# Optimization experiments

Hardware: AMD Instinct MI355X
Metric: run time of the kernel (lower is better)

Reference implementation:

```python
import jax, jax.numpy as jnp
from jax import lax
import numpy as np

WINDOW_SIZES = (1, 2, 3)


def _proj(x, w1, b1, w2, b2):
    # gated projection: sigmoid(Linear1) * tanh(Linear2)
    return jax.nn.sigmoid(x @ w1.T + b1) * jnp.tanh(x @ w2.T + b2)


def setup_inputs() -> dict:
    key = jax.random.key(0)
    ks = jax.random.split(key, 16)
    V, E, D = 50000, 1024, 1024
    N, La, Lq = 64, 512, 64
    s = 0.02  # weight scale to keep sigmoid/tanh unsaturated
    return {
        "data_q": jax.random.randint(ks[0], (Lq,), 0, V),
        "data_as": jax.random.randint(ks[1], (N, La), 0, V),
        "emb": jax.random.normal(ks[2], (V, E), jnp.float32),
        "w1": jax.random.normal(ks[3], (D, E), jnp.float32) * s,
        "b1": jnp.zeros((D,), jnp.float32),
        "w2": jax.random.normal(ks[4], (D, E), jnp.float32) * s,
        "b2": jnp.zeros((D,), jnp.float32),
        "cw1": jax.random.normal(ks[5], (D, D, 1), jnp.float32) * s,
        "cb1": jnp.zeros((D,), jnp.float32),
        "cw2": jax.random.normal(ks[6], (D, D, 2), jnp.float32) * s,
        "cb2": jnp.zeros((D,), jnp.float32),
        "cw3": jax.random.normal(ks[7], (D, D, 3), jnp.float32) * s,
        "cb3": jnp.zeros((D,), jnp.float32),
        "lin_w": jax.random.normal(ks[8], (D, 3 * D), jnp.float32) * s,
        "lin_b": jnp.zeros((D,), jnp.float32),
        "soft_w": jax.random.normal(ks[9], (1, D), jnp.float32) * s,
        "soft_b": jnp.zeros((1,), jnp.float32),
    }


def reference(data_q, data_as, emb, w1, b1, w2, b2,
              cw1, cb1, cw2, cb2, cw3, cb3, lin_w, lin_b, soft_w, soft_b):
    N, La = data_as.shape
    a_tok = data_as.reshape(-1)                     # [T] concatenated answers
    emb_a = emb[a_tok]                              # [T, E]
    emb_q = emb[data_q]                             # [Lq, E]
    pa = _proj(emb_a, w1, b1, w2, b2)               # [T, D]
    pq = _proj(emb_q, w1, b1, w2, b2)               # [Lq, D]

    # attention: M_r = q @ a^T ; alpha = softmax over question positions
    M = pq @ pa.T                                   # [Lq, T]
    alpha = jax.nn.softmax(M.T, axis=1)             # [T, Lq]
    Y = alpha @ pq                                  # [T, D]
    sim = pa * Y                                    # elementwise compare (mul)

    starts = jnp.arange(N) * La
    x = sim.T[None]                                 # [1, D, T]
    pools = []
    for w, cw, cb in zip(WINDOW_SIZES, (cw1, cw2, cw3), (cb1, cb2, cb3)):
        conv = lax.conv_general_dilated(
            x, cw, (1,), 'VALID',
            dimension_numbers=('NCW', 'OIW', 'NCW'))[0].T + cb  # [T-w+1, D]
        conv = jax.nn.relu(conv)
        # DMax: per-answer max over rows [start_k, start_k + La - w + 1)
        idx = starts[:, None] + jnp.arange(La - w + 1)[None, :]  # [N, La-w+1]
        pools.append(conv[idx].max(axis=1))          # [N, D]

    cat = jnp.concatenate(pools, axis=1)            # [N, 3D]
    h = jnp.tanh(cat @ lin_w.T + lin_b)             # [N, D]
    logits = (h @ soft_w.T + soft_b).reshape(-1)    # [N]
    return jax.nn.log_softmax(logits)
```

## Files before the change

### kernel.cpp

```cpp
#include <hip/hip_runtime.h>

#define DEV __device__ __forceinline__

typedef __bf16 bf16x8 __attribute__((ext_vector_type(8)));
typedef float f32x4 __attribute__((ext_vector_type(4)));
typedef unsigned short u16;
typedef u16 u16x4 __attribute__((ext_vector_type(4)));

constexpr int T_ANS = 32768;
constexpr int LQ    = 64;
constexpr int M_ALL = T_ANS + LQ;
constexpr int M_PAD = 32896;
constexpr int DIM   = 1024;

DEV u16 f2bf(float x) {
  unsigned u = __float_as_uint(x);
  return (u16)((u + 0x7FFFu + ((u >> 16) & 1u)) >> 16);
}
DEV float bf2f(u16 s) { return __uint_as_float(((unsigned)s) << 16); }

DEV void gl2lds16(const void* g, void* l) {
  __builtin_amdgcn_global_load_lds(
      (const __attribute__((address_space(1))) unsigned int*)g,
      (__attribute__((address_space(3))) unsigned int*)l, 16, 0, 0);
}


__global__ void cast4(const float* __restrict__ src, u16* __restrict__ dst, int n4) {
  int i = blockIdx.x * 256 + threadIdx.x;
  if (i < n4) {
    float4 v = ((const float4*)src)[i];
    u16x4 o = { f2bf(v.x), f2bf(v.y), f2bf(v.z), f2bf(v.w) };
    ((u16x4*)dst)[i] = o;
  }
}

template<int W>
__global__ void cast_conv_w(const float* __restrict__ src, u16* __restrict__ dst) {
  int i = blockIdx.x * 256 + threadIdx.x;
  if (i < 1024 * 1024) {
#pragma unroll
    for (int k = 0; k < W; ++k)
      dst[(size_t)k * (1024 * 1024) + i] = f2bf(src[(size_t)i * W + k]);
  }
}

__global__ void gather_cast(const int* __restrict__ dq, const int* __restrict__ das,
                            const float* __restrict__ emb, u16* __restrict__ X) {
  const int row = blockIdx.x;
  const int c   = threadIdx.x;
  size_t dsto = (size_t)row * DIM + c * 4;
  if (row >= M_ALL) {
    u16x4 z = {0, 0, 0, 0};
    *(u16x4*)(X + dsto) = z;
    return;
  }
  const int tok = (row < T_ANS) ? das[row] : dq[row - T_ANS];
  float4 v = ((const float4*)(emb + (size_t)tok * DIM))[c];
  u16x4 o = { f2bf(v.x), f2bf(v.y), f2bf(v.z), f2bf(v.w) };
  *(u16x4*)(X + dsto) = o;
}

__global__ void transpose_pq(const u16* __restrict__ pa, u16* __restrict__ pqT) {
  int i = blockIdx.x * 256 + threadIdx.x;
  int e = i >> 6, q = i & 63;
  pqT[i] = pa[(size_t)(T_ANS + q) * DIM + e];
}

__global__ void zero_pad_sim(u16* __restrict__ sim) {
  int i = blockIdx.x * 256 + threadIdx.x;
  if (i < 2 * DIM) sim[(size_t)T_ANS * DIM + i] = 0;
}

__global__ void cast_cat(const float* __restrict__ cat, u16* __restrict__ catb) {
  int i = blockIdx.x * 256 + threadIdx.x;
  if (i < 128 * 3072) {
    int row = i / 3072;
    catb[i] = (row < 64) ? f2bf(cat[i]) : (u16)0;
  }
}


__global__ __launch_bounds__(256, 2)
void proj_dual(const u16* __restrict__ X, const u16* __restrict__ B1,
               const u16* __restrict__ B2, const float* __restrict__ b1,
               const float* __restrict__ b2, u16* __restrict__ pa) {
  __shared__ alignas(16) u16 sA[128 * 32];
  __shared__ alignas(16) u16 sB1[128 * 32];
  __shared__ alignas(16) u16 sB2[128 * 32];
  const int tid = threadIdx.x, lane = tid & 63;
  const int tm = blockIdx.x * 128, tn = blockIdx.y * 128;
  const int wid = tid >> 6;
  const int wm = (wid >> 1) * 64, wn = (wid & 1) * 64;
  f32x4 acc1[4][4] = {}, acc2[4][4] = {};
  for (int k0 = 0; k0 < 1024; k0 += 32) {
#pragma unroll
    for (int j = 0; j < 2; ++j) {
      const int f = tid * 16 + j * 4096;
      const int r = f >> 6, cb = f & 63;
      gl2lds16((const char*)X  + (size_t)(tm + r) * 2048 + k0 * 2 + cb, (char*)sA  + f);
      gl2lds16((const char*)B1 + (size_t)(tn + r) * 2048 + k0 * 2 + cb, (char*)sB1 + f);
      gl2lds16((const char*)B2 + (size_t)(tn + r) * 2048 + k0 * 2 + cb, (char*)sB2 + f);
    }
    __syncthreads();
    const int lr = lane & 15, lk = (lane >> 4) * 8;
    bf16x8 af[4], bf1[4], bf2[4];
#pragma unroll
    for (int i = 0; i < 4; ++i) {
      af[i]  = *(const bf16x8*)(sA  + (wm + i * 16 + lr) * 32 + lk);
      bf1[i] = *(const bf16x8*)(sB1 + (wn + i * 16 + lr) * 32 + lk);
      bf2[i] = *(const bf16x8*)(sB2 + (wn + i * 16 + lr) * 32 + lk);
    }
#pragma unroll
    for (int mi = 0; mi < 4; ++mi)
#pragma unroll
      for (int ni = 0; ni < 4; ++ni) {
        acc1[mi][ni] = __builtin_amdgcn_mfma_f32_16x16x32_bf16(af[mi], bf1[ni], acc1[mi][ni], 0, 0, 0);
        acc2[mi][ni] = __builtin_amdgcn_mfma_f32_16x16x32_bf16(af[mi], bf2[ni], acc2[mi][ni], 0, 0, 0);
      }
    __syncthreads();
  }
  const int lr = lane & 15, lg = (lane >> 4) * 4;
#pragma unroll
  for (int ni = 0; ni < 4; ++ni) {
    const int col = tn + wn + ni * 16 + lr;
    const float b1v = b1[col], b2v = b2[col];
#pragma unroll
    for (int mi = 0; mi < 4; ++mi)
#pragma unroll
      for (int r = 0; r < 4; ++r) {
        const int row = tm + wm + mi * 16 + lg + r;
        const float x1 = acc1[mi][ni][r] + b1v;
        const float x2 = acc2[mi][ni][r] + b2v;
        const float sg = 1.f / (1.f + __expf(-x1));
        const float th = 2.f / (1.f + __expf(-2.f * x2)) - 1.f;
        pa[(size_t)row * DIM + col] = f2bf(sg * th);
      }
  }
}


__global__ __launch_bounds__(256, 2)
void attn_s(const u16* __restrict__ pa, float* __restrict__ S) {
  __shared__ alignas(16) u16 sA[128 * 32];
  __shared__ alignas(16) u16 sB[64 * 32];
  const int tid = threadIdx.x, lane = tid & 63;
  const int tm = blockIdx.x * 128;
  const int wid = tid >> 6;
  const int wm = (wid >> 1) * 64, wn = (wid & 1) * 32;
  const u16* pq = pa + (size_t)T_ANS * DIM;
  f32x4 acc[4][2] = {};
  for (int k0 = 0; k0 < 1024; k0 += 32) {
#pragma unroll
    for (int j = 0; j < 2; ++j) {
      const int f = tid * 16 + j * 4096;
      const int r = f >> 6, cb = f & 63;
      gl2lds16((const char*)pa + (size_t)(tm + r) * 2048 + k0 * 2 + cb, (char*)sA + f);
    }
    {
      const int f = tid * 16;
      const int r = f >> 6, cb = f & 63;
      gl2lds16((const char*)pq + (size_t)r * 2048 + k0 * 2 + cb, (char*)sB + f);
    }
    __syncthreads();
    const int lr = lane & 15, lk = (lane >> 4) * 8;
    bf16x8 af[4], bfr[2];
#pragma unroll
    for (int i = 0; i < 4; ++i)
      af[i] = *(const bf16x8*)(sA + (wm + i * 16 + lr) * 32 + lk);
#pragma unroll
    for (int i = 0; i < 2; ++i)
      bfr[i] = *(const bf16x8*)(sB + (wn + i * 16 + lr) * 32 + lk);
#pragma unroll
    for (int mi = 0; mi < 4; ++mi)
#pragma unroll
      for (int ni = 0; ni < 2; ++ni)
        acc[mi][ni] = __builtin_amdgcn_mfma_f32_16x16x32_bf16(af[mi], bfr[ni], acc[mi][ni], 0, 0, 0);
    __syncthreads();
  }
  const int lr = lane & 15, lg = (lane >> 4) * 4;
#pragma unroll
  for (int mi = 0; mi < 4; ++mi)
#pragma unroll
    for (int ni = 0; ni < 2; ++ni)
#pragma unroll
      for (int r = 0; r < 4; ++r) {
        const int row = tm + wm + mi * 16 + lg + r;
        const int col = wn + ni * 16 + lr;
        S[(size_t)row * 64 + col] = acc[mi][ni][r];
      }
}

__global__ void softmax64(const float* __restrict__ S, u16* __restrict__ alpha) {
  const int row = blockIdx.x * 4 + (threadIdx.x >> 6);
  const int lane = threadIdx.x & 63;
  const float v = S[(size_t)row * 64 + lane];
  float m = v;
#pragma unroll
  for (int o = 32; o > 0; o >>= 1) m = fmaxf(m, __shfl_xor(m, o));
  const float e = __expf(v - m);
  float s = e;
#pragma unroll
  for (int o = 32; o > 0; o >>= 1) s += __shfl_xor(s, o);
  alpha[(size_t)row * 64 + lane] = f2bf(e / s);
}


__global__ __launch_bounds__(256, 2)
void attn_y_sim(const u16* __restrict__ alpha, const u16* __restrict__ pqT,
                const u16* __restrict__ pa, u16* __restrict__ sim) {
  __shared__ alignas(16) u16 sA[128 * 32];
  __shared__ alignas(16) u16 sB[128 * 32];
  const int tid = threadIdx.x, lane = tid & 63;
  const int tm = blockIdx.x * 128, tn = blockIdx.y * 128;
  const int wid = tid >> 6;
  const int wm = (wid >> 1) * 64, wn = (wid & 1) * 64;
  f32x4 acc[4][4] = {};
  for (int k0 = 0; k0 < 64; k0 += 32) {
#pragma unroll
    for (int j = 0; j < 2; ++j) {
      const int f = tid * 16 + j * 4096;
      const int r = f >> 6, cb = f & 63;
      gl2lds16((const char*)alpha + (size_t)(tm + r) * 128 + k0 * 2 + cb, (char*)sA + f);
      gl2lds16((const char*)pqT   + (size_t)(tn + r) * 128 + k0 * 2 + cb, (char*)sB + f);
    }
    __syncthreads();
    const int lr = lane & 15, lk = (lane >> 4) * 8;
    bf16x8 af[4], bfr[4];
#pragma unroll
    for (int i = 0; i < 4; ++i) {
      af[i]  = *(const bf16x8*)(sA + (wm + i * 16 + lr) * 32 + lk);
      bfr[i] = *(const bf16x8*)(sB + (wn + i * 16 + lr) * 32 + lk);
    }
#pragma unroll
    for (int mi = 0; mi < 4; ++mi)
#pragma unroll
      for (int ni = 0; ni < 4; ++ni)
        acc[mi][ni] = __builtin_amdgcn_mfma_f32_16x16x32_bf16(af[mi], bfr[ni], acc[mi][ni], 0, 0, 0);
    __syncthreads();
  }
  const int lr = lane & 15, lg = (lane >> 4) * 4;
#pragma unroll
  for (int ni = 0; ni < 4; ++ni) {
    const int col = tn + wn + ni * 16 + lr;
#pragma unroll
    for (int mi = 0; mi < 4; ++mi)
#pragma unroll
      for (int r = 0; r < 4; ++r) {
        const int row = tm + wm + mi * 16 + lg + r;
        const size_t o = (size_t)row * DIM + col;
        sim[o] = f2bf(bf2f(pa[o]) * acc[mi][ni][r]);
      }
  }
}


template<int W>
__global__ __launch_bounds__(256, 2)
void conv_pool(const u16* __restrict__ sim, const u16* __restrict__ Bw,
               const float* __restrict__ cb, float* __restrict__ cat) {
  __shared__ alignas(16) u16 sA[(128 + W) * 32];
  __shared__ alignas(16) u16 sB[W][128 * 32];
  const int tid = threadIdx.x, lane = tid & 63;
  const int tm = blockIdx.x * 128, tn = blockIdx.y * 128;
  const int wid = tid >> 6;
  const int wm = (wid >> 1) * 64, wn = (wid & 1) * 64;
  f32x4 acc[4][4] = {};
  for (int k0 = 0; k0 < 1024; k0 += 32) {
#pragma unroll
    for (int j = 0; j < 2; ++j) {
      const int f = tid * 16 + j * 4096;
      const int r = f >> 6, cbo = f & 63;
      gl2lds16((const char*)sim + (size_t)(tm + r) * 2048 + k0 * 2 + cbo, (char*)sA + f);
#pragma unroll
      for (int k = 0; k < W; ++k)
        gl2lds16((const char*)Bw + (size_t)k * 2097152 + (size_t)(tn + r) * 2048 + k0 * 2 + cbo,
                 (char*)&sB[k][0] + f);
    }
    if (W > 1 && tid < (W - 1) * 4) {
      const int f = 8192 + tid * 16;
      const int r = f >> 6, cbo = f & 63;
      gl2lds16((const char*)sim + (size_t)(tm + r) * 2048 + k0 * 2 + cbo, (char*)sA + f);
    }
    __syncthreads();
    const int lr = lane & 15, lk = (lane >> 4) * 8;
#pragma unroll
    for (int k = 0; k < W; ++k) {
      bf16x8 af[4], bfr[4];
#pragma unroll
      for (int i = 0; i < 4; ++i) {
        af[i]  = *(const bf16x8*)(sA + (wm + i * 16 + lr + k) * 32 + lk);
        bfr[i] = *(const bf16x8*)(&sB[k][0] + (wn + i * 16 + lr) * 32 + lk);
      }
#pragma unroll
      for (int mi = 0; mi < 4; ++mi)
#pragma unroll
        for (int ni = 0; ni < 4; ++ni)
          acc[mi][ni] = __builtin_amdgcn_mfma_f32_16x16x32_bf16(af[mi], bfr[ni], acc[mi][ni], 0, 0, 0);
    }
    __syncthreads();
  }
  const int lr = lane & 15, lg = (lane >> 4) * 4;
  const int n = tm >> 9;
#pragma unroll
  for (int ni = 0; ni < 4; ++ni) {
    const int col = tn + wn + ni * 16 + lr;
    const float cbv = cb[col];
    float vmax = 0.f;
#pragma unroll
    for (int mi = 0; mi < 4; ++mi)
#pragma unroll
      for (int r = 0; r < 4; ++r) {
        const int t = tm + wm + mi * 16 + lg + r;
        float v = fmaxf(acc[mi][ni][r] + cbv, 0.f);
        if ((t & 511) > 512 - W) v = 0.f;
        vmax = fmaxf(vmax, v);
      }
    vmax = fmaxf(vmax, __shfl_xor(vmax, 16));
    vmax = fmaxf(vmax, __shfl_xor(vmax, 32));
    if (lane < 16)
      atomicMax((int*)&cat[(size_t)n * 3072 + (W - 1) * 1024 + col], __float_as_int(vmax));
  }
}


__global__ __launch_bounds__(256, 2)
void final_h(const u16* __restrict__ catb, const u16* __restrict__ linb,
             const float* __restrict__ lin_b, float* __restrict__ h) {
  __shared__ alignas(16) u16 sA[128 * 32];
  __shared__ alignas(16) u16 sB[128 * 32];
  const int tid = threadIdx.x, lane = tid & 63;
  const int tn = blockIdx.y * 128;
  const int wid = tid >> 6;
  const int wm = (wid >> 1) * 64, wn = (wid & 1) * 64;
  f32x4 acc[4][4] = {};
  for (int k0 = 0; k0 < 3072; k0 += 32) {
#pragma unroll
    for (int j = 0; j < 2; ++j) {
      const int f = tid * 16 + j * 4096;
      const int r = f >> 6, cb = f & 63;
      gl2lds16((const char*)catb + (size_t)r * 6144 + k0 * 2 + cb, (char*)sA + f);
      gl2lds16((const char*)linb + (size_t)(tn + r) * 6144 + k0 * 2 + cb, (char*)sB + f);
    }
    __syncthreads();
    const int lr = lane & 15, lk = (lane >> 4) * 8;
    bf16x8 af[4], bfr[4];
#pragma unroll
    for (int i = 0; i < 4; ++i) {
      af[i]  = *(const bf16x8*)(sA + (wm + i * 16 + lr) * 32 + lk);
      bfr[i] = *(const bf16x8*)(sB + (wn + i * 16 + lr) * 32 + lk);
    }
#pragma unroll
    for (int mi = 0; mi < 4; ++mi)
#pragma unroll
      for (int ni = 0; ni < 4; ++ni)
        acc[mi][ni] = __builtin_amdgcn_mfma_f32_16x16x32_bf16(af[mi], bfr[ni], acc[mi][ni], 0, 0, 0);
    __syncthreads();
  }
  const int lr = lane & 15, lg = (lane >> 4) * 4;
#pragma unroll
  for (int ni = 0; ni < 4; ++ni) {
    const int col = tn + wn + ni * 16 + lr;
    const float bv = lin_b[col];
#pragma unroll
    for (int mi = 0; mi < 4; ++mi)
#pragma unroll
      for (int r = 0; r < 4; ++r) {
        const int row = wm + mi * 16 + lg + r;
        if (row < 64) {
          const float x = acc[mi][ni][r] + bv;
          h[(size_t)row * DIM + col] = 2.f / (1.f + __expf(-2.f * x)) - 1.f;
        }
      }
  }
}

__global__ void final_logits(const float* __restrict__ h, const float* __restrict__ soft_w,
                             const float* __restrict__ soft_b, float* __restrict__ out) {
  __shared__ float part[256];
  const int t = threadIdx.x;
  const int n = t >> 2, q = t & 3;
  float s = 0.f;
  for (int j = q * 256; j < q * 256 + 256; ++j) s += h[(size_t)n * DIM + j] * soft_w[j];
  part[t] = s;
  __syncthreads();
  if (t < 64) {
    float logit = part[t * 4] + part[t * 4 + 1] + part[t * 4 + 2] + part[t * 4 + 3] + soft_b[0];
    float m = logit;
#pragma unroll
    for (int o = 32; o > 0; o >>= 1) m = fmaxf(m, __shfl_xor(m, o));
    float e = __expf(logit - m);
    float ssum = e;
#pragma unroll
    for (int o = 32; o > 0; o >>= 1) ssum += __shfl_xor(ssum, o);
    out[t] = (logit - m) - logf(ssum);
  }
}


extern "C" void kernel_launch(void* const* d_in, const int* in_sizes, int n_in,
                              void* d_out, int out_size, void* d_ws, size_t ws_size,
                              hipStream_t stream) {
  const int*   data_q  = (const int*)d_in[0];
  const int*   data_as = (const int*)d_in[1];
  const float* emb     = (const float*)d_in[2];
  const float* w1      = (const float*)d_in[3];
  const float* b1      = (const float*)d_in[4];
  const float* w2      = (const float*)d_in[5];
  const float* b2      = (const float*)d_in[6];
  const float* cw1     = (const float*)d_in[7];
  const float* cb1     = (const float*)d_in[8];
  const float* cw2     = (const float*)d_in[9];
  const float* cb2     = (const float*)d_in[10];
  const float* cw3     = (const float*)d_in[11];
  const float* cb3     = (const float*)d_in[12];
  const float* lin_w   = (const float*)d_in[13];
  const float* lin_b   = (const float*)d_in[14];
  const float* soft_w  = (const float*)d_in[15];
  const float* soft_b  = (const float*)d_in[16];
  float* out = (float*)d_out;

  u16* X     = (u16*)d_ws;
  u16* pa    = X    + (size_t)M_PAD * DIM;
  u16* w1b   = pa   + (size_t)M_PAD * DIM;
  u16* w2b   = w1b  + 1024 * 1024;
  u16* cwb   = w2b  + 1024 * 1024;
  u16* linb  = cwb  + (size_t)6 * 1024 * 1024;
  u16* pqT   = linb + (size_t)3 * 1024 * 1024;
  u16* alpha = pqT  + 64 * 1024;
  float* S   = (float*)(alpha + (size_t)T_ANS * 64);
  float* cat = S + (size_t)T_ANS * 64;
  u16* catb  = (u16*)(cat + 64 * 3072);
  float* h   = (float*)(catb + 128 * 3072);
  u16* simb  = X;

  hipMemsetAsync(cat, 0, 64 * 3072 * sizeof(float), stream);

  cast4<<<1024, 256, 0, stream>>>(w1, w1b, 1024 * 1024 / 4);
  cast4<<<1024, 256, 0, stream>>>(w2, w2b, 1024 * 1024 / 4);
  cast4<<<3072, 256, 0, stream>>>(lin_w, linb, 3072 * 1024 / 4);
  cast_conv_w<1><<<4096, 256, 0, stream>>>(cw1, cwb);
  cast_conv_w<2><<<4096, 256, 0, stream>>>(cw2, cwb + (size_t)1 * 1024 * 1024);
  cast_conv_w<3><<<4096, 256, 0, stream>>>(cw3, cwb + (size_t)3 * 1024 * 1024);

  gather_cast<<<M_PAD, 256, 0, stream>>>(data_q, data_as, emb, X);

  proj_dual<<<dim3(M_PAD / 128, 8), 256, 0, stream>>>(X, w1b, w2b, b1, b2, pa);
  transpose_pq<<<256, 256, 0, stream>>>(pa, pqT);

  attn_s<<<T_ANS / 128, 256, 0, stream>>>(pa, S);
  softmax64<<<T_ANS / 4, 256, 0, stream>>>(S, alpha);
  attn_y_sim<<<dim3(T_ANS / 128, 8), 256, 0, stream>>>(alpha, pqT, pa, simb);
  zero_pad_sim<<<8, 256, 0, stream>>>(simb);

  conv_pool<1><<<dim3(T_ANS / 128, 8), 256, 0, stream>>>(simb, cwb, cb1, cat);
  conv_pool<2><<<dim3(T_ANS / 128, 8), 256, 0, stream>>>(simb, cwb + (size_t)1 * 1024 * 1024, cb2, cat);
  conv_pool<3><<<dim3(T_ANS / 128, 8), 256, 0, stream>>>(simb, cwb + (size_t)3 * 1024 * 1024, cb3, cat);

  cast_cat<<<1536, 256, 0, stream>>>(cat, catb);
  final_h<<<dim3(1, 8), 256, 0, stream>>>(catb, linb, lin_b, h);
  final_logits<<<1, 256, 0, stream>>>(h, soft_w, soft_b, out);
}
```

Baseline: 855.6 us.

## Split-K attention scores and use 512-thread blocks for projection GEMM

The attention score GEMM is split four ways along K into partial buffers (reusing the dead X workspace), and the softmax kernel sums the four partials before normalising. This raises the grid from 256 blocks to 1024 so the CUs are better filled. The projection GEMM moves to 512 threads per block, each wave holding half the M rows, which cuts per-wave accumulator registers and adds waves to hide latency. In exchange it costs extra partial-sum memory traffic, and each wave now issues fewer MFMAs per LDS load.

```diff
diff --git a/kernel.cpp b/kernel.cpp
--- a/kernel.cpp
+++ b/kernel.cpp
@@ -81,7 +81,7 @@
 }
 
 
-__global__ __launch_bounds__(256, 2)
+__global__ __launch_bounds__(512, 2)
 void proj_dual(const u16* __restrict__ X, const u16* __restrict__ B1,
                const u16* __restrict__ B2, const float* __restrict__ b1,
                const float* __restrict__ b2, u16* __restrict__ pa) {
@@ -91,12 +91,11 @@
   const int tid = threadIdx.x, lane = tid & 63;
   const int tm = blockIdx.x * 128, tn = blockIdx.y * 128;
   const int wid = tid >> 6;
-  const int wm = (wid >> 1) * 64, wn = (wid & 1) * 64;
-  f32x4 acc1[4][4] = {}, acc2[4][4] = {};
+  const int wm = (wid >> 1) * 32, wn = (wid & 1) * 64;
+  f32x4 acc1[2][4] = {}, acc2[2][4] = {};
   for (int k0 = 0; k0 < 1024; k0 += 32) {
-#pragma unroll
-    for (int j = 0; j < 2; ++j) {
-      const int f = tid * 16 + j * 4096;
+    {
+      const int f = tid * 16;
       const int r = f >> 6, cb = f & 63;
       gl2lds16((const char*)X  + (size_t)(tm + r) * 2048 + k0 * 2 + cb, (char*)sA  + f);
       gl2lds16((const char*)B1 + (size_t)(tn + r) * 2048 + k0 * 2 + cb, (char*)sB1 + f);
@@ -104,19 +103,21 @@
     }
     __syncthreads();
     const int lr = lane & 15, lk = (lane >> 4) * 8;
-    bf16x8 af[4], bf1[4], bf2[4];
+    bf16x8 af[2], bv1[4], bv2[4];
+#pragma unroll
+    for (int i = 0; i < 2; ++i)
+      af[i]  = *(const bf16x8*)(sA  + (wm + i * 16 + lr) * 32 + lk);
 #pragma unroll
     for (int i = 0; i < 4; ++i) {
-      af[i]  = *(const bf16x8*)(sA  + (wm + i * 16 + lr) * 32 + lk);
-      bf1[i] = *(const bf16x8*)(sB1 + (wn + i * 16 + lr) * 32 + lk);
-      bf2[i] = *(const bf16x8*)(sB2 + (wn + i * 16 + lr) * 32 + lk);
-    }
-#pragma unroll
-    for (int mi = 0; mi < 4; ++mi)
+      bv1[i] = *(const bf16x8*)(sB1 + (wn + i * 16 + lr) * 32 + lk);
+      bv2[i] = *(const bf16x8*)(sB2 + (wn + i * 16 + lr) * 32 + lk);
+    }
+#pragma unroll
+    for (int mi = 0; mi < 2; ++mi)
 #pragma unroll
       for (int ni = 0; ni < 4; ++ni) {
-        acc1[mi][ni] = __builtin_amdgcn_mfma_f32_16x16x32_bf16(af[mi], bf1[ni], acc1[mi][ni], 0, 0, 0);
-        acc2[mi][ni] = __builtin_amdgcn_mfma_f32_16x16x32_bf16(af[mi], bf2[ni], acc2[mi][ni], 0, 0, 0);
+        acc1[mi][ni] = __builtin_amdgcn_mfma_f32_16x16x32_bf16(af[mi], bv1[ni], acc1[mi][ni], 0, 0, 0);
+        acc2[mi][ni] = __builtin_amdgcn_mfma_f32_16x16x32_bf16(af[mi], bv2[ni], acc2[mi][ni], 0, 0, 0);
       }
     __syncthreads();
   }
@@ -126,7 +127,7 @@
     const int col = tn + wn + ni * 16 + lr;
     const float b1v = b1[col], b2v = b2[col];
 #pragma unroll
-    for (int mi = 0; mi < 4; ++mi)
+    for (int mi = 0; mi < 2; ++mi)
 #pragma unroll
       for (int r = 0; r < 4; ++r) {
         const int row = tm + wm + mi * 16 + lg + r;
@@ -141,16 +142,17 @@
 
 
 __global__ __launch_bounds__(256, 2)
-void attn_s(const u16* __restrict__ pa, float* __restrict__ S) {
+void attn_s(const u16* __restrict__ pa, float* __restrict__ Spart) {
   __shared__ alignas(16) u16 sA[128 * 32];
   __shared__ alignas(16) u16 sB[64 * 32];
   const int tid = threadIdx.x, lane = tid & 63;
   const int tm = blockIdx.x * 128;
+  const int kbase = blockIdx.y * 256;
   const int wid = tid >> 6;
   const int wm = (wid >> 1) * 64, wn = (wid & 1) * 32;
   const u16* pq = pa + (size_t)T_ANS * DIM;
   f32x4 acc[4][2] = {};
-  for (int k0 = 0; k0 < 1024; k0 += 32) {
+  for (int k0 = kbase; k0 < kbase + 256; k0 += 32) {
 #pragma unroll
     for (int j = 0; j < 2; ++j) {
       const int f = tid * 16 + j * 4096;
@@ -179,6 +181,7 @@
     __syncthreads();
   }
   const int lr = lane & 15, lg = (lane >> 4) * 4;
+  float* Sp = Spart + (size_t)blockIdx.y * (T_ANS * 64);
 #pragma unroll
   for (int mi = 0; mi < 4; ++mi)
 #pragma unroll
@@ -187,21 +190,23 @@
       for (int r = 0; r < 4; ++r) {
         const int row = tm + wm + mi * 16 + lg + r;
         const int col = wn + ni * 16 + lr;
-        S[(size_t)row * 64 + col] = acc[mi][ni][r];
-      }
-}
-
-__global__ void softmax64(const float* __restrict__ S, u16* __restrict__ alpha) {
+        Sp[(size_t)row * 64 + col] = acc[mi][ni][r];
+      }
+}
+
+__global__ void softmax64(const float* __restrict__ Spart, u16* __restrict__ alpha) {
   const int row = blockIdx.x * 4 + (threadIdx.x >> 6);
   const int lane = threadIdx.x & 63;
-  const float v = S[(size_t)row * 64 + lane];
+  const size_t o = (size_t)row * 64 + lane;
+  float v = Spart[o] + Spart[(size_t)1 * T_ANS * 64 + o]
+          + Spart[(size_t)2 * T_ANS * 64 + o] + Spart[(size_t)3 * T_ANS * 64 + o];
   float m = v;
 #pragma unroll
-  for (int o = 32; o > 0; o >>= 1) m = fmaxf(m, __shfl_xor(m, o));
+  for (int o2 = 32; o2 > 0; o2 >>= 1) m = fmaxf(m, __shfl_xor(m, o2));
   const float e = __expf(v - m);
   float s = e;
 #pragma unroll
-  for (int o = 32; o > 0; o >>= 1) s += __shfl_xor(s, o);
+  for (int o2 = 32; o2 > 0; o2 >>= 1) s += __shfl_xor(s, o2);
   alpha[(size_t)row * 64 + lane] = f2bf(e / s);
 }
 
@@ -428,11 +433,12 @@
   u16* linb  = cwb  + (size_t)6 * 1024 * 1024;
   u16* pqT   = linb + (size_t)3 * 1024 * 1024;
   u16* alpha = pqT  + 64 * 1024;
-  float* S   = (float*)(alpha + (size_t)T_ANS * 64);
-  float* cat = S + (size_t)T_ANS * 64;
+  float* Sold= (float*)(alpha + (size_t)T_ANS * 64);
+  float* cat = Sold + (size_t)T_ANS * 64;
   u16* catb  = (u16*)(cat + 64 * 3072);
   float* h   = (float*)(catb + 128 * 3072);
   u16* simb  = X;
+  float* Spart = (float*)X;
 
   hipMemsetAsync(cat, 0, 64 * 3072 * sizeof(float), stream);
 
@@ -445,11 +451,11 @@
 
   gather_cast<<<M_PAD, 256, 0, stream>>>(data_q, data_as, emb, X);
 
-  proj_dual<<<dim3(M_PAD / 128, 8), 256, 0, stream>>>(X, w1b, w2b, b1, b2, pa);
+  proj_dual<<<dim3(M_PAD / 128, 8), 512, 0, stream>>>(X, w1b, w2b, b1, b2, pa);
   transpose_pq<<<256, 256, 0, stream>>>(pa, pqT);
 
-  attn_s<<<T_ANS / 128, 256, 0, stream>>>(pa, S);
-  softmax64<<<T_ANS / 4, 256, 0, stream>>>(S, alpha);
+  attn_s<<<dim3(T_ANS / 128, 4), 256, 0, stream>>>(pa, Spart);
+  softmax64<<<T_ANS / 4, 256, 0, stream>>>(Spart, alpha);
   attn_y_sim<<<dim3(T_ANS / 128, 8), 256, 0, stream>>>(alpha, pqT, pa, simb);
   zero_pad_sim<<<8, 256, 0, stream>>>(simb);
 
```

After: 865.1 us. Within noise of the previous version (+1.1%).
